# Optimization experiments

Hardware: AMD Instinct MI355X
Metric: run time of the kernel (lower is better)

Reference implementation:

```python
import jax, jax.numpy as jnp
import numpy as np

B, N, C = 32, 512, 1024
H = 16
D = C // H  # 64
MAX_SEQ = 512
BASE = 10000.0


def _rope_tables(n, d):
    # sin/cos tables of shape (n, d//2), matching the torch RoPE buffer math
    position = jnp.arange(n, dtype=jnp.float32)[:, None]
    div_term = jnp.exp(jnp.arange(0, d, 2, dtype=jnp.float32) * (-np.log(BASE) / d))
    ang = position * div_term
    return jnp.sin(ang), jnp.cos(ang)


def _apply_rope(x, sin, cos):
    # x: (B, H, N, D); sin/cos: (N, D//2)
    x1 = x[..., ::2]
    x2 = x[..., 1::2]
    out = jnp.stack([x1 * cos - x2 * sin, x1 * sin + x2 * cos], axis=-1)
    return out.reshape(*x.shape[:-1], -1)


def setup_inputs() -> dict:
    key = jax.random.key(0)
    k1, k2, k3, k4, k5 = jax.random.split(key, 5)
    s = 0.02
    return {
        "x": jax.random.normal(k1, (B, N, C), dtype=jnp.float32),
        "w_qkv": jax.random.normal(k2, (3 * C, C), dtype=jnp.float32) * s,
        "b_qkv": jax.random.normal(k3, (3 * C,), dtype=jnp.float32) * s,
        "w_lepe": jax.random.normal(k4, (C, 1, 3), dtype=jnp.float32) * s,
        "b_lepe": jax.random.normal(k5, (C,), dtype=jnp.float32) * s,
    }


def reference(x, w_qkv, b_qkv, w_lepe, b_lepe):
    b, n, c = x.shape
    scale = 1.0 / np.sqrt(D)
    sin, cos = _rope_tables(n, D)

    # fused QKV projection: (B,N,3C) -> (3,B,H,N,D)
    qkv = (x @ w_qkv.T + b_qkv).reshape(b, n, 3, H, D).transpose(2, 0, 3, 1, 4)
    q, k, v = qkv[0], qkv[1], qkv[2]

    # elu + 1 feature map
    q = jax.nn.elu(q) + 1.0
    k = jax.nn.elu(k) + 1.0

    # RoPE on q/k
    q = _apply_rope(q, sin, cos)
    k = _apply_rope(k, sin, cos)

    # explicit softmax attention
    attn = jnp.einsum('bhnd,bhmd->bhnm', q, k) * scale
    attn = jax.nn.softmax(attn, axis=-1)
    attn_out = jnp.einsum('bhnm,bhmd->bhnd', attn, v)  # (B,H,N,D)
    attn_out = attn_out.transpose(0, 2, 1, 3).reshape(b, n, c)

    # LePE: depthwise conv1d (k=3, pad=1, groups=C) on v reshaped to (B,C,N)
    v_conv = v.transpose(0, 2, 1, 3).reshape(b, n, c).transpose(0, 2, 1)
    lepe = jax.lax.conv_general_dilated(
        v_conv, w_lepe, window_strides=(1,), padding=((1, 1),),
        dimension_numbers=('NCH', 'OIH', 'NCH'), feature_group_count=c,
    ) + b_lepe[None, :, None]
    lepe = lepe.transpose(0, 2, 1)

    return attn_out + lepe
```

## Files before the change

kernel.cpp:

```cpp
#include <hip/hip_runtime.h>
#include <stdint.h>

typedef __attribute__((ext_vector_type(8))) __bf16 bf16x8;
typedef __attribute__((ext_vector_type(4))) float f32x4;
typedef __attribute__((ext_vector_type(8))) unsigned short u16x8;
typedef __attribute__((ext_vector_type(4))) unsigned short u16x4;

#define MFMA16(a, b, c) __builtin_amdgcn_mfma_f32_16x16x32_bf16((a), (b), (c), 0, 0, 0)

__device__ __forceinline__ void glds16(const void* g, void* l) {
  __builtin_amdgcn_global_load_lds(
      (const __attribute__((address_space(1))) void*)(uintptr_t)g,
      (__attribute__((address_space(3))) void*)(uint32_t)(uintptr_t)l,
      16, 0, 0);
}

__device__ __forceinline__ unsigned short f2bf(float f) {
  union { float f; unsigned u; } v; v.f = f;
  unsigned r = v.u + 0x7FFFu + ((v.u >> 16) & 1u);
  return (unsigned short)(r >> 16);
}
__device__ __forceinline__ float bf2f(unsigned short s) {
  union { unsigned u; float f; } v; v.u = ((unsigned)s) << 16;
  return v.f;
}
__device__ __forceinline__ bf16x8 as_bf16x8(u16x8 v) {
  union { u16x8 u; bf16x8 b; } c; c.u = v; return c.b;
}

#define B_ 32
#define N_ 512
#define C_ 1024
#define H_ 16
#define D_ 64
#define K_ C_

#define NX8 2097152
#define NW8 393216
#define NT8 2048

__global__ __launch_bounds__(256) void prep_kernel(
    const float* __restrict__ x, const float* __restrict__ w,
    unsigned short* __restrict__ xb, unsigned short* __restrict__ wb,
    float2* __restrict__ sc_t) {
  const int i = blockIdx.x * 256 + threadIdx.x;
  if (i < NX8 + NW8) {
    const float* src = (i < NX8) ? x : w;
    unsigned short* dst = (i < NX8) ? xb : wb;
    const int k = (i < NX8) ? i : i - NX8;
    const float4* p = reinterpret_cast<const float4*>(src) + (size_t)k * 2;
    float4 a = p[0], b = p[1];
    u16x8 o;
    o[0] = f2bf(a.x); o[1] = f2bf(a.y); o[2] = f2bf(a.z); o[3] = f2bf(a.w);
    o[4] = f2bf(b.x); o[5] = f2bf(b.y); o[6] = f2bf(b.z); o[7] = f2bf(b.w);
    *reinterpret_cast<u16x8*>(dst + (size_t)k * 8) = o;
  } else if (i < NX8 + NW8 + NT8) {
    const int base = (i - NX8 - NW8) * 8;
#pragma unroll
    for (int e = 0; e < 8; ++e) {
      const int idx = base + e;
      const int n = idx >> 5, ip = idx & 31;
      const float div = expf(-(2.0f * (float)ip) * (9.210340371976184f / 64.0f));
      const float ang = (float)n * div;
      sc_t[idx] = make_float2(sinf(ang), cosf(ang));
    }
  }
}

#define STAGE_T(bi, uu)                                                \
  do {                                                                 \
    _Pragma("unroll") for (int h_ = 0; h_ < 4; ++h_) {                 \
      glds16(aS[h_] + (size_t)(uu) * 64, &lds[bi][h_ * 4096 + t * 8]); \
      glds16(bS[h_] + (size_t)(uu) * 64,                               \
             &lds[bi][16384 + h_ * 4096 + t * 8]);                     \
    }                                                                  \
  } while (0)

__global__ __launch_bounds__(512, 2) void qkv_gemm_kernel(
    const unsigned short* __restrict__ xb, const unsigned short* __restrict__ wb,
    const float* __restrict__ bias,
    unsigned short* __restrict__ Qb, unsigned short* __restrict__ Kb,
    unsigned short* __restrict__ Vtb,
    const float2* __restrict__ sc_t) {
  __shared__ unsigned short lds[2][32768];
  const int t = threadIdx.x;
  const int wv = t >> 6, l = t & 63;
  const int wr = wv >> 2, wc = wv & 3;
  const int lq = l >> 4, lr = l & 15;

  const int bid = (blockIdx.x & 7) * 96 + (blockIdx.x >> 3);
  const int mBlk = bid / 12, nBlk = bid % 12;
  const int m0 = mBlk * 256, n0 = nBlk * 256;

  const int rl = t >> 3;
  const int cw = ((t & 7) ^ (rl & 7)) * 8;
  const unsigned short* aS[4];
  const unsigned short* bS[4];
#pragma unroll
  for (int h = 0; h < 4; ++h) {
    aS[h] = xb + (size_t)(m0 + h * 64 + rl) * K_ + cw;
    bS[h] = wb + (size_t)(n0 + h * 64 + rl) * K_ + cw;
  }

  const int aBase = (wr * 128 + lr) * 64;
  const int bBase = 16384 + (wc * 64 + lr) * 64;
  int chs[2];
#pragma unroll
  for (int s = 0; s < 2; ++s) chs[s] = ((s * 4 + lq) ^ (lr & 7)) * 8;

  f32x4 acc[8][4] = {};

  STAGE_T(0, 0);
  asm volatile("s_waitcnt vmcnt(0)" ::: "memory");
  __builtin_amdgcn_s_barrier();

  for (int u = 0; u < 16; ++u) {
    const int cur = u & 1;
    const unsigned short* Lc = &lds[cur][0];
    if (u + 1 < 16) STAGE_T(cur ^ 1, u + 1);

    bf16x8 afr[8][2], bfr[4][2];
#pragma unroll
    for (int mf = 0; mf < 8; ++mf)
#pragma unroll
      for (int s = 0; s < 2; ++s)
        afr[mf][s] = *(const bf16x8*)(Lc + aBase + mf * 1024 + chs[s]);
#pragma unroll
    for (int j = 0; j < 4; ++j)
#pragma unroll
      for (int s = 0; s < 2; ++s)
        bfr[j][s] = *(const bf16x8*)(Lc + bBase + j * 1024 + chs[s]);

#pragma unroll
    for (int mf = 0; mf < 8; ++mf)
#pragma unroll
      for (int j = 0; j < 4; ++j)
#pragma unroll
        for (int s = 0; s < 2; ++s)
          acc[mf][j] = MFMA16(afr[mf][s], bfr[j][s], acc[mf][j]);

    asm volatile("s_waitcnt vmcnt(0)\n\ts_barrier" ::: "memory");
  }

  if (n0 >= 2048) {
#pragma unroll
    for (int mf = 0; mf < 8; ++mf) {
#pragma unroll
      for (int j = 0; j < 4; ++j) {
        const int ncol = n0 + wc * 64 + j * 16 + lr;
        const int hh = (ncol & 1023) >> 6;
        const int d = j * 16 + lr;
        const float bias_v = bias[ncol];
        const int m = m0 + wr * 128 + mf * 16 + lq * 4;
        const int bb = m >> 9, nB = m & 511;
        u16x4 vv;
#pragma unroll
        for (int r = 0; r < 4; ++r) vv[r] = f2bf(acc[mf][j][r] + bias_v);
        *(u16x4*)(Vtb + ((size_t)(bb * H_ + hh) * D_ + d) * N_ + nB) = vv;
      }
    }
  } else {
    const bool isQ = (n0 < 1024);
#pragma unroll
    for (int mf = 0; mf < 8; ++mf) {
#pragma unroll
      for (int j = 0; j < 4; ++j) {
        const int ncol = n0 + wc * 64 + j * 16 + lr;
        const int hh = (ncol & 1023) >> 6;
        const int d = ncol & 63;
        const float bias_v = bias[ncol];
        const int ip = d >> 1;
#pragma unroll
        for (int r = 0; r < 4; ++r) {
          const int m = m0 + wr * 128 + mf * 16 + lq * 4 + r;
          const int bb = m >> 9, n = m & 511;
          const float val = acc[mf][j][r] + bias_v;
          const float e = val > 0.f ? val + 1.f : expf(val);
          const float partner = __shfl_xor(e, 1);
          const float2 sc = sc_t[n * 32 + ip];
          float o = (d & 1) ? (partner * sc.x + e * sc.y) : (e * sc.y - partner * sc.x);
          if (isQ) o *= 0.125f;
          unsigned short* dst = isQ ? Qb : Kb;
          dst[((size_t)(bb * H_ + hh) * N_ + n) * D_ + d] = f2bf(o);
        }
      }
    }
  }
}

__global__ __launch_bounds__(512, 2) void attn_kernel(
    const unsigned short* __restrict__ Qb, const unsigned short* __restrict__ Kb,
    const unsigned short* __restrict__ Vtb,
    const float* __restrict__ w_lepe, const float* __restrict__ b_lepe,
    float* __restrict__ out) {
  __shared__ unsigned short Ks[512 * 64];
  __shared__ unsigned short Vs[64 * 512];
  __shared__ unsigned short Pb[8 * 2 * 1024];
  const int t = threadIdx.x, wv = t >> 6, l = t & 63;
  const int lq = l >> 4, lr = l & 15;
  const int bh = blockIdx.x;
  const int bb = bh >> 4, h = bh & 15;
  const size_t base = (size_t)bh * (N_ * D_);

  {
    const int row8 = t >> 3, ch = t & 7;
#pragma unroll
    for (int c = 0; c < 8; ++c) {
      const int r = c * 64 + row8;
      const int sch = ch ^ (r & 7);
      glds16(Kb + base + (size_t)r * D_ + sch * 8, Ks + c * 4096 + t * 8);
    }
  }
  {
    const int ch = t & 63;
#pragma unroll
    for (int c = 0; c < 8; ++c) {
      const int d = c * 8 + wv;
      const int sch = ch ^ (d & 7);
      glds16(Vtb + base + (size_t)d * N_ + sch * 8, Vs + c * 4096 + t * 8);
    }
  }

  asm volatile("s_waitcnt vmcnt(8)" ::: "memory");
  __builtin_amdgcn_s_barrier();

  unsigned short* PwA = Pb + wv * 2048;
  unsigned short* PwB = PwA + 1024;

#define PWRITE(ccv, Pdst)                                                        \
  do {                                                                           \
    _Pragma("unroll") for (int kl = 0; kl < 4; ++kl) {                           \
      const int kt_ = (ccv) * 4 + kl;                                            \
      u16x4 pk;                                                                  \
      _Pragma("unroll") for (int r = 0; r < 4; ++r) pk[r] = f2bf(s[kt_][r] * inv); \
      const int slot = kl * 2 + (lq >> 1);                                       \
      *(u16x4*)((Pdst) + lr * 64 + ((slot ^ (lr & 7)) << 3) + (lq & 1) * 4) = pk; \
    }                                                                            \
  } while (0)

  bf16x8 qf0 = *(const bf16x8*)(Qb + base + (size_t)(wv * 64 + lr) * D_ + lq * 8);
  bf16x8 qf1 = *(const bf16x8*)(Qb + base + (size_t)(wv * 64 + lr) * D_ + 32 + lq * 8);

  for (int p = 0; p < 4; ++p) {
    const int ql = wv * 64 + p * 16;

    f32x4 s[32];
#pragma unroll
    for (int kt = 0; kt < 32; ++kt) {
      const int r = kt * 16 + lr;
      const int rx = r & 7;
      const unsigned short* kr = Ks + r * 64;
      const bf16x8 kf0 = *(const bf16x8*)(kr + (lq ^ rx) * 8);
      const bf16x8 kf1 = *(const bf16x8*)(kr + ((lq + 4) ^ rx) * 8);
      f32x4 a = {0.f, 0.f, 0.f, 0.f};
      a = MFMA16(kf0, qf0, a);
      a = MFMA16(kf1, qf1, a);
      s[kt] = a;
    }

    if (p < 3) {
      const int qn = ql + 16;
      qf0 = *(const bf16x8*)(Qb + base + (size_t)(qn + lr) * D_ + lq * 8);
      qf1 = *(const bf16x8*)(Qb + base + (size_t)(qn + lr) * D_ + 32 + lq * 8);
    }

    float macc[8];
#pragma unroll
    for (int i = 0; i < 8; ++i) macc[i] = -1e30f;
#pragma unroll
    for (int kt = 0; kt < 32; ++kt)
#pragma unroll
      for (int r = 0; r < 4; ++r)
        macc[(kt & 1) * 4 + r] = fmaxf(macc[(kt & 1) * 4 + r], s[kt][r]);
#pragma unroll
    for (int i = 0; i < 4; ++i) macc[i] = fmaxf(macc[i], macc[i + 4]);
    macc[0] = fmaxf(macc[0], macc[1]);
    macc[2] = fmaxf(macc[2], macc[3]);
    float m = fmaxf(macc[0], macc[2]);
    m = fmaxf(m, __shfl_xor(m, 16));
    m = fmaxf(m, __shfl_xor(m, 32));

    float sacc[8];
#pragma unroll
    for (int i = 0; i < 8; ++i) sacc[i] = 0.f;
#pragma unroll
    for (int kt = 0; kt < 32; ++kt)
#pragma unroll
      for (int r = 0; r < 4; ++r) {
        const float pv = __expf(s[kt][r] - m);
        s[kt][r] = pv;
        sacc[(kt & 1) * 4 + r] += pv;
      }
#pragma unroll
    for (int i = 0; i < 4; ++i) sacc[i] += sacc[i + 4];
    sacc[0] += sacc[1];
    sacc[2] += sacc[3];
    float su = sacc[0] + sacc[2];
    su += __shfl_xor(su, 16);
    su += __shfl_xor(su, 32);
    const float inv = 1.0f / su;

    if (p == 0) __syncthreads();

    f32x4 o[4] = {};
    PWRITE(0, PwA);
#pragma unroll
    for (int cc = 0; cc < 8; ++cc) {
      unsigned short* bufC = (cc & 1) ? PwB : PwA;
      unsigned short* bufN = (cc & 1) ? PwA : PwB;
      if (cc < 7) PWRITE(cc + 1, bufN);
      asm volatile("s_waitcnt lgkmcnt(4)" ::: "memory");
#pragma unroll
      for (int w = 0; w < 2; ++w) {
        const u16x8 pr =
            *(const u16x8*)(bufC + lr * 64 + (((w * 4 + lq) ^ (lr & 7)) << 3));
        const bf16x8 pf = as_bf16x8(pr);
        const int ci = cc * 8 + w * 4 + lq;
#pragma unroll
        for (int j2 = 0; j2 < 4; j2++) {
          const int dr = j2 * 16 + lr;
          const bf16x8 vf = *(const bf16x8*)(Vs + dr * 512 + ((ci ^ (dr & 7)) << 3));
          o[j2] = MFMA16(pf, vf, o[j2]);
        }
      }
    }

#pragma unroll
    for (int j2 = 0; j2 < 4; j2++) {
      const int d = j2 * 16 + lr;
      const int c = h * 64 + d;
      const float w0 = w_lepe[c * 3 + 0], w1 = w_lepe[c * 3 + 1], w2 = w_lepe[c * 3 + 2];
      const float bl = b_lepe[c];
      const int dx = d & 7;
#pragma unroll
      for (int r = 0; r < 4; r++) {
        const int n = ql + lq * 4 + r;
        float vm1 = 0.f, vp1 = 0.f;
        if (n > 0) {
          const int nn = n - 1;
          vm1 = bf2f(Vs[d * 512 + (((nn >> 3) ^ dx) << 3) + (nn & 7)]);
        }
        const float v0 = bf2f(Vs[d * 512 + (((n >> 3) ^ dx) << 3) + (n & 7)]);
        if (n < 511) {
          const int nn = n + 1;
          vp1 = bf2f(Vs[d * 512 + (((nn >> 3) ^ dx) << 3) + (nn & 7)]);
        }
        const float lepe = vm1 * w0 + v0 * w1 + vp1 * w2 + bl;
        out[((size_t)(bb * N_ + n)) * C_ + c] = o[j2][r] + lepe;
      }
    }
  }
#undef PWRITE
}

extern "C" void kernel_launch(void* const* d_in, const int* in_sizes, int n_in,
                              void* d_out, int out_size, void* d_ws, size_t ws_size,
                              hipStream_t stream) {
  (void)in_sizes; (void)n_in; (void)out_size; (void)ws_size;
  const float* x = (const float*)d_in[0];
  const float* w_qkv = (const float*)d_in[1];
  const float* b_qkv = (const float*)d_in[2];
  const float* w_lepe = (const float*)d_in[3];
  const float* b_lepe = (const float*)d_in[4];
  float* out = (float*)d_out;

  unsigned short* ws = (unsigned short*)d_ws;
  unsigned short* xb = ws;
  unsigned short* wb = xb + 16777216;
  unsigned short* Qb = wb + 3145728;
  unsigned short* Kb = Qb + 16777216;
  unsigned short* Vtb = Kb + 16777216;
  float2* sc_t = (float2*)(Vtb + 16777216);

  const int prep_units = NX8 + NW8 + NT8;
  prep_kernel<<<(prep_units + 255) / 256, 256, 0, stream>>>(x, w_qkv, xb, wb, sc_t);
  qkv_gemm_kernel<<<768, 512, 0, stream>>>(xb, wb, b_qkv, Qb, Kb, Vtb, sc_t);
  attn_kernel<<<512, 512, 0, stream>>>(Qb, Kb, Vtb, w_lepe, b_lepe, out);
}
```

Measured before the change: 232.5 us.

## Process two heads per attention block and prefetch next head's K/V into LDS

The attention kernel now launches half as many blocks, with each block handling two (batch, head) pairs in sequence. The next head's K tile is staged into LDS during the last query pass of the first head, and its V tile right after the first head finishes. The goal is to overlap global-to-LDS loads with compute and to amortize block launch and setup. In exchange, fewer blocks means less parallelism: 256 blocks may leave CUs idle or unbalanced on a GPU with many CUs, and the extra barriers add serialization.

```diff
diff --git a/kernel.cpp b/kernel.cpp
--- a/kernel.cpp
+++ b/kernel.cpp
@@ -198,29 +198,31 @@
   __shared__ unsigned short Pb[8 * 2 * 1024];
   const int t = threadIdx.x, wv = t >> 6, l = t & 63;
   const int lq = l >> 4, lr = l & 15;
-  const int bh = blockIdx.x;
-  const int bb = bh >> 4, h = bh & 15;
-  const size_t base = (size_t)bh * (N_ * D_);
-
-  {
-    const int row8 = t >> 3, ch = t & 7;
-#pragma unroll
-    for (int c = 0; c < 8; ++c) {
-      const int r = c * 64 + row8;
-      const int sch = ch ^ (r & 7);
-      glds16(Kb + base + (size_t)r * D_ + sch * 8, Ks + c * 4096 + t * 8);
-    }
-  }
-  {
-    const int ch = t & 63;
-#pragma unroll
-    for (int c = 0; c < 8; ++c) {
-      const int d = c * 8 + wv;
-      const int sch = ch ^ (d & 7);
-      glds16(Vtb + base + (size_t)d * N_ + sch * 8, Vs + c * 4096 + t * 8);
-    }
-  }
-
+  const int bid = blockIdx.x;
+
+#define STAGE_K(gbase)                                                     \
+  do {                                                                     \
+    const int row8_ = t >> 3, ch_ = t & 7;                                 \
+    _Pragma("unroll") for (int c_ = 0; c_ < 8; ++c_) {                     \
+      const int r_ = c_ * 64 + row8_;                                      \
+      const int sch_ = ch_ ^ (r_ & 7);                                     \
+      glds16(Kb + (gbase) + (size_t)r_ * D_ + sch_ * 8,                    \
+             Ks + c_ * 4096 + t * 8);                                      \
+    }                                                                      \
+  } while (0)
+#define STAGE_V(gbase)                                                     \
+  do {                                                                     \
+    const int ch_ = t & 63;                                                \
+    _Pragma("unroll") for (int c_ = 0; c_ < 8; ++c_) {                     \
+      const int d_ = c_ * 8 + wv;                                          \
+      const int sch_ = ch_ ^ (d_ & 7);                                     \
+      glds16(Vtb + (gbase) + (size_t)d_ * N_ + sch_ * 8,                   \
+             Vs + c_ * 4096 + t * 8);                                      \
+    }                                                                      \
+  } while (0)
+
+  STAGE_K((size_t)(bid * 2) * (N_ * D_));
+  STAGE_V((size_t)(bid * 2) * (N_ * D_));
   asm volatile("s_waitcnt vmcnt(8)" ::: "memory");
   __builtin_amdgcn_s_barrier();
 
@@ -238,119 +240,141 @@
     }                                                                            \
   } while (0)
 
-  bf16x8 qf0 = *(const bf16x8*)(Qb + base + (size_t)(wv * 64 + lr) * D_ + lq * 8);
-  bf16x8 qf1 = *(const bf16x8*)(Qb + base + (size_t)(wv * 64 + lr) * D_ + 32 + lq * 8);
-
-  for (int p = 0; p < 4; ++p) {
-    const int ql = wv * 64 + p * 16;
-
-    f32x4 s[32];
-#pragma unroll
-    for (int kt = 0; kt < 32; ++kt) {
-      const int r = kt * 16 + lr;
-      const int rx = r & 7;
-      const unsigned short* kr = Ks + r * 64;
-      const bf16x8 kf0 = *(const bf16x8*)(kr + (lq ^ rx) * 8);
-      const bf16x8 kf1 = *(const bf16x8*)(kr + ((lq + 4) ^ rx) * 8);
-      f32x4 a = {0.f, 0.f, 0.f, 0.f};
-      a = MFMA16(kf0, qf0, a);
-      a = MFMA16(kf1, qf1, a);
-      s[kt] = a;
+  for (int bhi = 0; bhi < 2; ++bhi) {
+    const int bh = bid * 2 + bhi;
+    const int bb = bh >> 4, h = bh & 15;
+    const size_t base = (size_t)bh * (N_ * D_);
+    const size_t base2 = base + (size_t)(N_ * D_);
+
+    bf16x8 qf0 = *(const bf16x8*)(Qb + base + (size_t)(wv * 64 + lr) * D_ + lq * 8);
+    bf16x8 qf1 = *(const bf16x8*)(Qb + base + (size_t)(wv * 64 + lr) * D_ + 32 + lq * 8);
+
+    for (int p = 0; p < 4; ++p) {
+      const int ql = wv * 64 + p * 16;
+
+      f32x4 s[32];
+#pragma unroll
+      for (int kt = 0; kt < 32; ++kt) {
+        const int r = kt * 16 + lr;
+        const int rx = r & 7;
+        const unsigned short* kr = Ks + r * 64;
+        const bf16x8 kf0 = *(const bf16x8*)(kr + (lq ^ rx) * 8);
+        const bf16x8 kf1 = *(const bf16x8*)(kr + ((lq + 4) ^ rx) * 8);
+        f32x4 a = {0.f, 0.f, 0.f, 0.f};
+        a = MFMA16(kf0, qf0, a);
+        a = MFMA16(kf1, qf1, a);
+        s[kt] = a;
+      }
+
+      if (p == 3 && bhi == 0) {
+        __syncthreads();
+        STAGE_K(base2);
+      }
+
+      if (p < 3) {
+        const int qn = ql + 16;
+        qf0 = *(const bf16x8*)(Qb + base + (size_t)(qn + lr) * D_ + lq * 8);
+        qf1 = *(const bf16x8*)(Qb + base + (size_t)(qn + lr) * D_ + 32 + lq * 8);
+      }
+
+      float macc[8];
+#pragma unroll
+      for (int i = 0; i < 8; ++i) macc[i] = -1e30f;
+#pragma unroll
+      for (int kt = 0; kt < 32; ++kt)
+#pragma unroll
+        for (int r = 0; r < 4; ++r)
+          macc[(kt & 1) * 4 + r] = fmaxf(macc[(kt & 1) * 4 + r], s[kt][r]);
+#pragma unroll
+      for (int i = 0; i < 4; ++i) macc[i] = fmaxf(macc[i], macc[i + 4]);
+      macc[0] = fmaxf(macc[0], macc[1]);
+      macc[2] = fmaxf(macc[2], macc[3]);
+      float m = fmaxf(macc[0], macc[2]);
+      m = fmaxf(m, __shfl_xor(m, 16));
+      m = fmaxf(m, __shfl_xor(m, 32));
+
+      float sacc[8];
+#pragma unroll
+      for (int i = 0; i < 8; ++i) sacc[i] = 0.f;
+#pragma unroll
+      for (int kt = 0; kt < 32; ++kt)
+#pragma unroll
+        for (int r = 0; r < 4; ++r) {
+          const float pv = __expf(s[kt][r] - m);
+          s[kt][r] = pv;
+          sacc[(kt & 1) * 4 + r] += pv;
+        }
+#pragma unroll
+      for (int i = 0; i < 4; ++i) sacc[i] += sacc[i + 4];
+      sacc[0] += sacc[1];
+      sacc[2] += sacc[3];
+      float su = sacc[0] + sacc[2];
+      su += __shfl_xor(su, 16);
+      su += __shfl_xor(su, 32);
+      const float inv = 1.0f / su;
+
+      if (p == 0) __syncthreads();
+
+      f32x4 o[4] = {};
+      PWRITE(0, PwA);
+#pragma unroll
+      for (int cc = 0; cc < 8; ++cc) {
+        unsigned short* bufC = (cc & 1) ? PwB : PwA;
+        unsigned short* bufN = (cc & 1) ? PwA : PwB;
+        if (cc < 7) PWRITE(cc + 1, bufN);
+        asm volatile("s_waitcnt lgkmcnt(4)" ::: "memory");
+#pragma unroll
+        for (int w = 0; w < 2; ++w) {
+          const u16x8 pr =
+              *(const u16x8*)(bufC + lr * 64 + (((w * 4 + lq) ^ (lr & 7)) << 3));
+          const bf16x8 pf = as_bf16x8(pr);
+          const int ci = cc * 8 + w * 4 + lq;
+#pragma unroll
+          for (int j2 = 0; j2 < 4; j2++) {
+            const int dr = j2 * 16 + lr;
+            const bf16x8 vf = *(const bf16x8*)(Vs + dr * 512 + ((ci ^ (dr & 7)) << 3));
+            o[j2] = MFMA16(pf, vf, o[j2]);
+          }
+        }
+      }
+
+#pragma unroll
+      for (int j2 = 0; j2 < 4; j2++) {
+        const int d = j2 * 16 + lr;
+        const int c = h * 64 + d;
+        const float w0 = w_lepe[c * 3 + 0], w1 = w_lepe[c * 3 + 1],
+                    w2 = w_lepe[c * 3 + 2];
+        const float bl = b_lepe[c];
+        const int dx = d & 7;
+#pragma unroll
+        for (int r = 0; r < 4; r++) {
+          const int n = ql + lq * 4 + r;
+          float vm1 = 0.f, vp1 = 0.f;
+          if (n > 0) {
+            const int nn = n - 1;
+            vm1 = bf2f(Vs[d * 512 + (((nn >> 3) ^ dx) << 3) + (nn & 7)]);
+          }
+          const float v0 = bf2f(Vs[d * 512 + (((n >> 3) ^ dx) << 3) + (n & 7)]);
+          if (n < 511) {
+            const int nn = n + 1;
+            vp1 = bf2f(Vs[d * 512 + (((nn >> 3) ^ dx) << 3) + (nn & 7)]);
+          }
+          const float lepe = vm1 * w0 + v0 * w1 + vp1 * w2 + bl;
+          out[((size_t)(bb * N_ + n)) * C_ + c] = o[j2][r] + lepe;
+        }
+      }
     }
 
-    if (p < 3) {
-      const int qn = ql + 16;
-      qf0 = *(const bf16x8*)(Qb + base + (size_t)(qn + lr) * D_ + lq * 8);
-      qf1 = *(const bf16x8*)(Qb + base + (size_t)(qn + lr) * D_ + 32 + lq * 8);
-    }
-
-    float macc[8];
-#pragma unroll
-    for (int i = 0; i < 8; ++i) macc[i] = -1e30f;
-#pragma unroll
-    for (int kt = 0; kt < 32; ++kt)
-#pragma unroll
-      for (int r = 0; r < 4; ++r)
-        macc[(kt & 1) * 4 + r] = fmaxf(macc[(kt & 1) * 4 + r], s[kt][r]);
-#pragma unroll
-    for (int i = 0; i < 4; ++i) macc[i] = fmaxf(macc[i], macc[i + 4]);
-    macc[0] = fmaxf(macc[0], macc[1]);
-    macc[2] = fmaxf(macc[2], macc[3]);
-    float m = fmaxf(macc[0], macc[2]);
-    m = fmaxf(m, __shfl_xor(m, 16));
-    m = fmaxf(m, __shfl_xor(m, 32));
-
-    float sacc[8];
-#pragma unroll
-    for (int i = 0; i < 8; ++i) sacc[i] = 0.f;
-#pragma unroll
-    for (int kt = 0; kt < 32; ++kt)
-#pragma unroll
-      for (int r = 0; r < 4; ++r) {
-        const float pv = __expf(s[kt][r] - m);
-        s[kt][r] = pv;
-        sacc[(kt & 1) * 4 + r] += pv;
-      }
-#pragma unroll
-    for (int i = 0; i < 4; ++i) sacc[i] += sacc[i + 4];
-    sacc[0] += sacc[1];
-    sacc[2] += sacc[3];
-    float su = sacc[0] + sacc[2];
-    su += __shfl_xor(su, 16);
-    su += __shfl_xor(su, 32);
-    const float inv = 1.0f / su;
-
-    if (p == 0) __syncthreads();
-
-    f32x4 o[4] = {};
-    PWRITE(0, PwA);
-#pragma unroll
-    for (int cc = 0; cc < 8; ++cc) {
-      unsigned short* bufC = (cc & 1) ? PwB : PwA;
-      unsigned short* bufN = (cc & 1) ? PwA : PwB;
-      if (cc < 7) PWRITE(cc + 1, bufN);
-      asm volatile("s_waitcnt lgkmcnt(4)" ::: "memory");
-#pragma unroll
-      for (int w = 0; w < 2; ++w) {
-        const u16x8 pr =
-            *(const u16x8*)(bufC + lr * 64 + (((w * 4 + lq) ^ (lr & 7)) << 3));
-        const bf16x8 pf = as_bf16x8(pr);
-        const int ci = cc * 8 + w * 4 + lq;
-#pragma unroll
-        for (int j2 = 0; j2 < 4; j2++) {
-          const int dr = j2 * 16 + lr;
-          const bf16x8 vf = *(const bf16x8*)(Vs + dr * 512 + ((ci ^ (dr & 7)) << 3));
-          o[j2] = MFMA16(pf, vf, o[j2]);
-        }
-      }
-    }
-
-#pragma unroll
-    for (int j2 = 0; j2 < 4; j2++) {
-      const int d = j2 * 16 + lr;
-      const int c = h * 64 + d;
-      const float w0 = w_lepe[c * 3 + 0], w1 = w_lepe[c * 3 + 1], w2 = w_lepe[c * 3 + 2];
-      const float bl = b_lepe[c];
-      const int dx = d & 7;
-#pragma unroll
-      for (int r = 0; r < 4; r++) {
-        const int n = ql + lq * 4 + r;
-        float vm1 = 0.f, vp1 = 0.f;
-        if (n > 0) {
-          const int nn = n - 1;
-          vm1 = bf2f(Vs[d * 512 + (((nn >> 3) ^ dx) << 3) + (nn & 7)]);
-        }
-        const float v0 = bf2f(Vs[d * 512 + (((n >> 3) ^ dx) << 3) + (n & 7)]);
-        if (n < 511) {
-          const int nn = n + 1;
-          vp1 = bf2f(Vs[d * 512 + (((nn >> 3) ^ dx) << 3) + (nn & 7)]);
-        }
-        const float lepe = vm1 * w0 + v0 * w1 + vp1 * w2 + bl;
-        out[((size_t)(bb * N_ + n)) * C_ + c] = o[j2][r] + lepe;
-      }
+    if (bhi == 0) {
+      __syncthreads();
+      STAGE_V(base2);
+      asm volatile("s_waitcnt vmcnt(8)" ::: "memory");
+      __builtin_amdgcn_s_barrier();
     }
   }
 #undef PWRITE
+#undef STAGE_K
+#undef STAGE_V
 }
 
 extern "C" void kernel_launch(void* const* d_in, const int* in_sizes, int n_in,
@@ -375,5 +399,5 @@
   const int prep_units = NX8 + NW8 + NT8;
   prep_kernel<<<(prep_units + 255) / 256, 256, 0, stream>>>(x, w_qkv, xb, wb, sc_t);
   qkv_gemm_kernel<<<768, 512, 0, stream>>>(xb, wb, b_qkv, Qb, Kb, Vtb, sc_t);
-  attn_kernel<<<512, 512, 0, stream>>>(Qb, Kb, Vtb, w_lepe, b_lepe, out);
-}
+  attn_kernel<<<256, 512, 0, stream>>>(Qb, Kb, Vtb, w_lepe, b_lepe, out);
+}
```

Result: no change. 236.2 us (+1.6%).

## Triple-buffer A tiles in QKV GEMM with a single barrier per iteration

Applied to the files above, without the earlier changes.

Restructures the QKV GEMM main loop so A tiles are triple-buffered and B tiles double-buffered in a larger shared LDS array. Each iteration now has one barrier with a partial vmcnt wait, so the next A tile can stay in flight while the current tile is consumed. The aim is to overlap global-to-LDS loads with MFMA work and remove the trailing full drain and barrier. It also replaces expf with the faster __expf in the ELU epilogue. LDS use rises to 160 KB per block, which limits occupancy to one block per CU.

```diff
diff --git a/kernel.cpp b/kernel.cpp
--- a/kernel.cpp
+++ b/kernel.cpp
@@ -67,13 +67,17 @@
   }
 }
 
-#define STAGE_T(bi, uu)                                                \
+#define STAGE_A(dstoff, uu)                                            \
   do {                                                                 \
-    _Pragma("unroll") for (int h_ = 0; h_ < 4; ++h_) {                 \
-      glds16(aS[h_] + (size_t)(uu) * 64, &lds[bi][h_ * 4096 + t * 8]); \
+    _Pragma("unroll") for (int h_ = 0; h_ < 4; ++h_)                   \
+      glds16(aS[h_] + (size_t)(uu) * 64,                               \
+             &lds[(dstoff) + h_ * 4096 + t * 8]);                      \
+  } while (0)
+#define STAGE_B(dstoff, uu)                                            \
+  do {                                                                 \
+    _Pragma("unroll") for (int h_ = 0; h_ < 4; ++h_)                   \
       glds16(bS[h_] + (size_t)(uu) * 64,                               \
-             &lds[bi][16384 + h_ * 4096 + t * 8]);                     \
-    }                                                                  \
+             &lds[(dstoff) + h_ * 4096 + t * 8]);                      \
   } while (0)
 
 __global__ __launch_bounds__(512, 2) void qkv_gemm_kernel(
@@ -82,7 +86,7 @@
     unsigned short* __restrict__ Qb, unsigned short* __restrict__ Kb,
     unsigned short* __restrict__ Vtb,
     const float2* __restrict__ sc_t) {
-  __shared__ unsigned short lds[2][32768];
+  __shared__ unsigned short lds[81920];
   const int t = threadIdx.x;
   const int wv = t >> 6, l = t & 63;
   const int wr = wv >> 2, wc = wv & 3;
@@ -103,33 +107,41 @@
   }
 
   const int aBase = (wr * 128 + lr) * 64;
-  const int bBase = 16384 + (wc * 64 + lr) * 64;
+  const int bBase = (wc * 64 + lr) * 64;
   int chs[2];
 #pragma unroll
   for (int s = 0; s < 2; ++s) chs[s] = ((s * 4 + lq) ^ (lr & 7)) * 8;
 
   f32x4 acc[8][4] = {};
 
-  STAGE_T(0, 0);
-  asm volatile("s_waitcnt vmcnt(0)" ::: "memory");
-  __builtin_amdgcn_s_barrier();
+  STAGE_A(0, 0);
+  STAGE_B(49152, 0);
+  STAGE_A(16384, 1);
+
+  int aCur = 0, aNx1 = 16384, aNx2 = 32768;
+  int bCur = 49152, bNxt = 65536;
 
   for (int u = 0; u < 16; ++u) {
-    const int cur = u & 1;
-    const unsigned short* Lc = &lds[cur][0];
-    if (u + 1 < 16) STAGE_T(cur ^ 1, u + 1);
-
+    if (u == 15) asm volatile("s_waitcnt vmcnt(0)" ::: "memory");
+    else         asm volatile("s_waitcnt vmcnt(4)" ::: "memory");
+    __builtin_amdgcn_s_barrier();
+
+    if (u + 1 < 16) STAGE_B(bNxt, u + 1);
+    if (u + 2 < 16) STAGE_A(aNx2, u + 2);
+
+    const unsigned short* La = &lds[aCur];
+    const unsigned short* Lb = &lds[bCur];
     bf16x8 afr[8][2], bfr[4][2];
 #pragma unroll
     for (int mf = 0; mf < 8; ++mf)
 #pragma unroll
       for (int s = 0; s < 2; ++s)
-        afr[mf][s] = *(const bf16x8*)(Lc + aBase + mf * 1024 + chs[s]);
+        afr[mf][s] = *(const bf16x8*)(La + aBase + mf * 1024 + chs[s]);
 #pragma unroll
     for (int j = 0; j < 4; ++j)
 #pragma unroll
       for (int s = 0; s < 2; ++s)
-        bfr[j][s] = *(const bf16x8*)(Lc + bBase + j * 1024 + chs[s]);
+        bfr[j][s] = *(const bf16x8*)(Lb + bBase + j * 1024 + chs[s]);
 
 #pragma unroll
     for (int mf = 0; mf < 8; ++mf)
@@ -139,7 +151,10 @@
         for (int s = 0; s < 2; ++s)
           acc[mf][j] = MFMA16(afr[mf][s], bfr[j][s], acc[mf][j]);
 
-    asm volatile("s_waitcnt vmcnt(0)\n\ts_barrier" ::: "memory");
+    const int aOld = aCur;
+    aCur = aNx1; aNx1 = aNx2; aNx2 = aOld;
+    const int bOld = bCur;
+    bCur = bNxt; bNxt = bOld;
   }
 
   if (n0 >= 2048) {
@@ -175,7 +190,7 @@
           const int m = m0 + wr * 128 + mf * 16 + lq * 4 + r;
           const int bb = m >> 9, n = m & 511;
           const float val = acc[mf][j][r] + bias_v;
-          const float e = val > 0.f ? val + 1.f : expf(val);
+          const float e = val > 0.f ? val + 1.f : __expf(val);
           const float partner = __shfl_xor(e, 1);
           const float2 sc = sc_t[n * 32 + ip];
           float o = (d & 1) ? (partner * sc.x + e * sc.y) : (e * sc.y - partner * sc.x);
```

Result: faster. 224.8 us (-3.3%).
